# Optimization experiments

Measured on AMD Instinct MI355X. Metric: run time of the kernel, lower is better.

## Reference

```python
import jax, jax.numpy as jnp
import numpy as np

D = 256; H = 4; HD = 64; NL = 12; MAXP = 16; DIM = 8; PDIM = 4; B = 128
EPS = 1e-5
SCALE = float(np.sqrt(HD))


def _ln(x, g, b):
    m = jnp.mean(x, -1, keepdims=True)
    v = jnp.mean((x - m) ** 2, -1, keepdims=True)
    return (x - m) * jax.lax.rsqrt(v + EPS) * g + b


def _mha(xq, xkv, Wqkv, bqkv, Wo, bo, causal):
    # Wqkv is the packed PyTorch in_proj_weight [3D, D]
    Bq, S, _ = xq.shape
    K = xkv.shape[1]
    q = (xq @ Wqkv[:D].T + bqkv[:D]).reshape(Bq, S, H, HD).transpose(0, 2, 1, 3)
    k = (xkv @ Wqkv[D:2 * D].T + bqkv[D:2 * D]).reshape(Bq, K, H, HD).transpose(0, 2, 1, 3)
    v = (xkv @ Wqkv[2 * D:].T + bqkv[2 * D:]).reshape(Bq, K, H, HD).transpose(0, 2, 1, 3)
    s = jnp.einsum('bhqd,bhkd->bhqk', q, k) / SCALE
    if causal:
        s = jnp.where(jnp.tril(jnp.ones((S, K), bool)), s, -jnp.inf)
    a = jax.nn.softmax(s, -1)
    o = jnp.einsum('bhqk,bhkd->bhqd', a, v).transpose(0, 2, 1, 3).reshape(Bq, S, D)
    return o @ Wo.T + bo


def _decode(tgt, mem, p):
    # post-LN TransformerDecoder (norm_first=False), dropout in eval mode
    x = tgt
    for l in range(NL):
        x = _ln(x + _mha(x, x, p['sa_Wqkv'][l], p['sa_bqkv'][l], p['sa_Wo'][l], p['sa_bo'][l], True), p['ln1_g'][l], p['ln1_b'][l])
        x = _ln(x + _mha(x, mem, p['ca_Wqkv'][l], p['ca_bqkv'][l], p['ca_Wo'][l], p['ca_bo'][l], False), p['ln2_g'][l], p['ln2_b'][l])
        h = jax.nn.relu(x @ p['lin1_W'][l].T + p['lin1_b'][l])
        x = _ln(x + h @ p['lin2_W'][l].T + p['lin2_b'][l], p['ln3_g'][l], p['ln3_b'][l])
    return x


def _forward(U_real, U_imag, tok_W, tok_b, pos_emb, sa_Wqkv, sa_bqkv, sa_Wo, sa_bo, ca_Wqkv, ca_bqkv, ca_Wo, ca_bo, lin1_W, lin1_b, lin2_W, lin2_b, ln1_g, ln1_b, ln2_g, ln2_b, ln3_g, ln3_b, out_W, out_b, param_low, param_high):
    p = dict(sa_Wqkv=sa_Wqkv, sa_bqkv=sa_bqkv, sa_Wo=sa_Wo, sa_bo=sa_bo,
             ca_Wqkv=ca_Wqkv, ca_bqkv=ca_bqkv, ca_Wo=ca_Wo, ca_bo=ca_bo,
             lin1_W=lin1_W, lin1_b=lin1_b, lin2_W=lin2_W, lin2_b=lin2_b,
             ln1_g=ln1_g, ln1_b=ln1_b, ln2_g=ln2_g, ln2_b=ln2_b, ln3_g=ln3_g, ln3_b=ln3_b)
    Bq = U_real.shape[0]
    vec = jnp.concatenate([U_real.reshape(Bq, -1), U_imag.reshape(Bq, -1)], -1)  # [B, 2*dim^2]
    src = vec @ tok_W.T + tok_b  # [B, D]
    mem = src[:, None, :]  # [B, 1, D] cross-attn memory
    seq = [src]
    for i in range(MAXP):
        tgt = jnp.stack(seq, 1) + pos_emb[:i + 1][None]  # [B, i+1, D]
        x = _decode(tgt, mem, p)
        seq.append(x[:, -1])
    logits = jnp.stack(seq[1:], 1)  # [B, MAXP, D]
    pn = jax.nn.sigmoid(logits @ out_W.T + out_b)  # [B, MAXP, PDIM]
    return param_low + (param_high - param_low) * pn


def setup_inputs() -> dict:
    key = jax.random.key(0)
    ks = jax.random.split(key, 16)
    def w(k, shape, s=0.02):
        return jax.random.normal(k, shape, dtype=jnp.float32) * s
    return {
        'U_real': jax.random.normal(ks[0], (B, DIM, DIM), dtype=jnp.float32),
        'U_imag': jax.random.normal(ks[1], (B, DIM, DIM), dtype=jnp.float32),
        'tok_W': w(ks[2], (D, 2 * DIM * DIM)), 'tok_b': jnp.zeros((D,), jnp.float32),
        'pos_emb': w(ks[3], (MAXP + 1, D)),
        'sa_Wqkv': w(ks[4], (NL, 3 * D, D)), 'sa_bqkv': jnp.zeros((NL, 3 * D), jnp.float32),
        'sa_Wo': w(ks[5], (NL, D, D)), 'sa_bo': jnp.zeros((NL, D), jnp.float32),
        'ca_Wqkv': w(ks[6], (NL, 3 * D, D)), 'ca_bqkv': jnp.zeros((NL, 3 * D), jnp.float32),
        'ca_Wo': w(ks[7], (NL, D, D)), 'ca_bo': jnp.zeros((NL, D), jnp.float32),
        'lin1_W': w(ks[8], (NL, 4 * D, D)), 'lin1_b': jnp.zeros((NL, 4 * D), jnp.float32),
        'lin2_W': w(ks[9], (NL, D, 4 * D)), 'lin2_b': jnp.zeros((NL, D), jnp.float32),
        'ln1_g': jnp.ones((NL, D), jnp.float32), 'ln1_b': jnp.zeros((NL, D), jnp.float32),
        'ln2_g': jnp.ones((NL, D), jnp.float32), 'ln2_b': jnp.zeros((NL, D), jnp.float32),
        'ln3_g': jnp.ones((NL, D), jnp.float32), 'ln3_b': jnp.zeros((NL, D), jnp.float32),
        'out_W': w(ks[10], (PDIM, D)), 'out_b': jnp.zeros((PDIM,), jnp.float32),
        'param_low': jnp.array([-1.0, 0.0, 0.0, 0.0], jnp.float32),
        'param_high': jnp.array([1.0, 1.0, 6.2832, 1.0], jnp.float32),
    }


def reference(U_real, U_imag, tok_W, tok_b, pos_emb, sa_Wqkv, sa_bqkv, sa_Wo, sa_bo, ca_Wqkv, ca_bqkv, ca_Wo, ca_bo, lin1_W, lin1_b, lin2_W, lin2_b, ln1_g, ln1_b, ln2_g, ln2_b, ln3_g, ln3_b, out_W, out_b, param_low, param_high):
    return _forward(U_real, U_imag, tok_W, tok_b, pos_emb, sa_Wqkv, sa_bqkv, sa_Wo, sa_bo, ca_Wqkv, ca_bqkv, ca_Wo, ca_bo, lin1_W, lin1_b, lin2_W, lin2_b, ln1_g, ln1_b, ln2_g, ln2_b, ln3_g, ln3_b, out_W, out_b, param_low, param_high)
```

## Files before the change

### kernel.cpp

```cpp
#include <hip/hip_runtime.h>
#include <hip/hip_bf16.h>


typedef __attribute__((ext_vector_type(8))) short short8;
typedef __attribute__((ext_vector_type(4))) float f32x4;

#define EPS_ 1e-5f

__device__ __forceinline__ unsigned short f2b(float x){
  union { float f; unsigned u; } c; c.f = x;
  unsigned r = (c.u + 0x7fffu + ((c.u >> 16) & 1u)) >> 16;
  return (unsigned short)r;
}
__device__ __forceinline__ float b2f(unsigned short u){
  union { unsigned u; float f; } c; c.u = ((unsigned)u) << 16;
  return c.f;
}
__device__ __forceinline__ unsigned long long pack4b(const f32x4 a){
  return (unsigned long long)f2b(a[0]) |
         ((unsigned long long)f2b(a[1]) << 16) |
         ((unsigned long long)f2b(a[2]) << 32) |
         ((unsigned long long)f2b(a[3]) << 48);
}
__device__ __forceinline__ unsigned long long pack2f(float a, float b){
  union { float f; unsigned u; } x, y; x.f = a; y.f = b;
  return (unsigned long long)x.u | ((unsigned long long)y.u << 32);
}
__device__ __forceinline__ float lo_f(unsigned long long v){
  union { unsigned u; float f; } c; c.u = (unsigned)v; return c.f;
}
__device__ __forceinline__ float hi_f(unsigned long long v){
  union { unsigned u; float f; } c; c.u = (unsigned)(v >> 32); return c.f;
}

#define AL(p)    __hip_atomic_load((p),  __ATOMIC_RELAXED, __HIP_MEMORY_SCOPE_AGENT)
#define AS(p,v)  __hip_atomic_store((p), (v), __ATOMIC_RELAXED, __HIP_MEMORY_SCOPE_AGENT)

#define OFF_WQKV 0ull
#define OFF_WO   4718592ull
#define OFF_L1   6291456ull
#define OFF_L2   12582912ull
#define OFF_SRC  18874368ull
#define OFF_CC   19005440ull
#define OFF_KV   19791872ull
#define OFF_XH   44957696ull
#define OFF_ZA   45219840ull
#define OFF_ZB   45613056ull
#define OFF_FLG  46006272ull

__global__ void k_conv(const float* __restrict__ wqkv, const float* __restrict__ wo,
                       const float* __restrict__ l1, const float* __restrict__ l2,
                       unsigned short* __restrict__ dst){
  const long long n0 = 12LL*768*256;
  const long long n1 = n0 + 12LL*256*256;
  const long long n2 = n1 + 12LL*1024*256;
  const long long n3 = n2 + 12LL*256*1024;
  for (long long idx = (long long)blockIdx.x*256 + threadIdx.x; idx < n3;
       idx += (long long)gridDim.x*256){
    float v;
    if (idx < n0) v = wqkv[idx];
    else if (idx < n1) v = wo[idx - n0];
    else if (idx < n2) v = l1[idx - n1];
    else v = l2[idx - n2];
    dst[idx] = f2b(v);
  }
}

__global__ void k_src(const float* __restrict__ U_real, const float* __restrict__ U_imag,
                      const float* __restrict__ tok_W, const float* __restrict__ tok_b,
                      const float* __restrict__ pos,
                      float* __restrict__ src, float* __restrict__ xh0){
  int b = blockIdx.x, n = threadIdx.x;
  const float* w = tok_W + n*128;
  const float* ur = U_real + b*64;
  const float* ui = U_imag + b*64;
  float acc = tok_b[n];
  #pragma unroll 8
  for (int k = 0; k < 64; ++k) acc += w[k]*ur[k];
  #pragma unroll 8
  for (int k = 0; k < 64; ++k) acc += w[64+k]*ui[k];
  src[b*256+n] = acc;
  xh0[b*256+n] = acc + pos[n];
}

__global__ void k_cc(const float* __restrict__ caW, const float* __restrict__ cab,
                     const float* __restrict__ caWo, const float* __restrict__ cabo,
                     const float* __restrict__ src, unsigned short* __restrict__ cc){
  int l = blockIdx.x >> 7, b = blockIdx.x & 127, t = threadIdx.x;
  __shared__ float v[256];
  const float* s = src + b*256;
  {
    const float* w = caW + ((long long)l*768 + 512 + t)*256;
    float a = cab[l*768 + 512 + t];
    #pragma unroll 8
    for (int k = 0; k < 256; ++k) a += w[k]*s[k];
    v[t] = a;
  }
  __syncthreads();
  {
    const float* w = caWo + ((long long)l*256 + t)*256;
    float a = cabo[l*256 + t];
    #pragma unroll 8
    for (int k = 0; k < 256; ++k) a += w[k]*v[k];
    cc[((long long)l*128 + b)*256 + t] = f2b(a);
  }
}

#define PUBW(FARR) do{                                                       \
  __syncthreads();                                                           \
  if (tid == 0) AS(FARR + l*4 + h, seq);                                     \
  if (tid < 3){                                                              \
    int ho = tid + (tid >= h ? 1 : 0);                                       \
    const int* fp = FARR + l*4 + ho;                                         \
    while (AL(fp) < seq) __builtin_amdgcn_s_sleep(2);                        \
  }                                                                          \
  __syncthreads();                                                           \
}while(0)

__global__ __launch_bounds__(512, 1) void k_main(
  const unsigned short* __restrict__ wqkv,
  const unsigned short* __restrict__ wo,
  const unsigned short* __restrict__ wl1,
  const unsigned short* __restrict__ wl2,
  const float* __restrict__ bqkv, const float* __restrict__ bo_,
  const float* __restrict__ bl1,  const float* __restrict__ bl2,
  const float* __restrict__ g1, const float* __restrict__ be1,
  const float* __restrict__ g2, const float* __restrict__ be2,
  const float* __restrict__ g3, const float* __restrict__ be3,
  const unsigned short* __restrict__ cc,
  const float* __restrict__ pos,
  const float* __restrict__ outW,
  const float* __restrict__ outb,
  const float* __restrict__ plow, const float* __restrict__ phigh,
  unsigned short* __restrict__ kvc,
  unsigned long long* __restrict__ xh,
  unsigned long long* __restrict__ zA,
  unsigned long long* __restrict__ zB,
  int* __restrict__ flags,
  float* __restrict__ out)
{
  __shared__ float xf[16][260];
  __shared__ float zf[16][260];
  __shared__ float yf[16][260];
  __shared__ unsigned short xb[16][264];
  __shared__ unsigned short hs[16][264];
  __shared__ unsigned short qs[16][72];
  __shared__ unsigned short os[16][72];

  const int tid  = threadIdx.x;
  const int w    = tid >> 6, lane = tid & 63;
  const int l    = blockIdx.x >> 2;
  const int h    = blockIdx.x & 3;
  const int mrow = lane & 15, kgrp = lane >> 4;

  int* fin = flags;
  int* fA  = flags + 384;
  int* fB  = flags + 432;

  for (int t = 0; t < 16; ++t){
    for (int g = 0; g < 8; ++g){
      const int seq = t*8 + g + 1;

      {
        int need = (l == 0) ? t : (t+1);
        if (need > 0 && tid < 4){
          const int* fp = fin + (l*4 + tid)*8 + g;
          while (AL(fp) < need) __builtin_amdgcn_s_sleep(2);
        }
        __syncthreads();
        int row = tid >> 5, c8 = (tid & 31)*8;
        const unsigned long long* xp =
            xh + (((size_t)(l & 1)*8 + g)*16 + row)*128 + (c8 >> 1);
        #pragma unroll
        for (int j = 0; j < 4; ++j){
          unsigned long long v = AL(xp + j);
          float f0 = lo_f(v), f1 = hi_f(v);
          xf[row][c8+2*j]   = f0;  xf[row][c8+2*j+1] = f1;
          xb[row][c8+2*j]   = f2b(f0);
          xb[row][c8+2*j+1] = f2b(f1);
        }
      }
      __syncthreads();

      {
        short8 a[8];
        #pragma unroll
        for (int kc = 0; kc < 8; ++kc)
          a[kc] = *(const short8*)&xb[mrow][kc*32 + kgrp*8];
        const unsigned short* wl = wqkv + (size_t)l*196608;
        for (int t2 = w; t2 < 12; t2 += 8){
          int p = t2 >> 2, q4 = t2 & 3;
          int n_l = q4*16 + mrow;
          const unsigned short* wp = wl + (size_t)(p*256 + h*64 + n_l)*256 + kgrp*8;
          f32x4 acc = {0,0,0,0};
          #pragma unroll
          for (int kc = 0; kc < 8; ++kc){
            short8 b0 = *(const short8*)(wp + kc*32);
            acc = __builtin_amdgcn_mfma_f32_16x16x32_bf16(a[kc], b0, acc, 0,0,0);
          }
          float bias = bqkv[l*768 + p*256 + h*64 + n_l];
          #pragma unroll
          for (int r = 0; r < 4; ++r){
            int br = kgrp*4 + r;
            float v = acc[r] + bias;
            if (p == 0){
              qs[br][n_l] = f2b(v);
            } else {
              size_t kb = (((((size_t)l*4 + h)*8 + g)*16 + br)*16 + t)*128
                          + (p == 2 ? 64 : 0) + n_l;
              kvc[kb] = f2b(v);
            }
          }
        }
      }
      __syncthreads();

      {
        int row = w*2 + (lane >> 5);
        int lid = lane & 31;
        float q0 = b2f(qs[row][lid*2]), q1 = b2f(qs[row][lid*2+1]);
        const unsigned short* base =
            kvc + (((((size_t)l*4 + h)*8 + g)*16 + row)*16)*128 + lid*2;
        float sv[16];
        #pragma unroll
        for (int j = 0; j < 16; ++j){
          if (j <= t){
            const unsigned short* kp = base + j*128;
            float p = q0*b2f(kp[0]) + q1*b2f(kp[1]);
            p += __shfl_xor(p, 1);
            p += __shfl_xor(p, 2);
            p += __shfl_xor(p, 4);
            p += __shfl_xor(p, 8);
            p += __shfl_xor(p, 16);
            sv[j] = p * 0.125f;
          } else sv[j] = -1e30f;
        }
        float mx = sv[0];
        #pragma unroll
        for (int j = 1; j < 16; ++j) mx = fmaxf(mx, sv[j]);
        float den = 0.f, e[16];
        #pragma unroll
        for (int j = 0; j < 16; ++j){ e[j] = __expf(sv[j]-mx); den += e[j]; }
        float rd = 1.f/den;
        float o0 = 0.f, o1 = 0.f;
        #pragma unroll
        for (int j = 0; j < 16; ++j){
          if (j <= t){
            const unsigned short* vp = base + j*128 + 64;
            o0 += e[j]*b2f(vp[0]);
            o1 += e[j]*b2f(vp[1]);
          }
        }
        os[row][lid*2]   = f2b(o0*rd);
        os[row][lid*2+1] = f2b(o1*rd);
      }
      __syncthreads();

      {
        short8 a2[2];
        #pragma unroll
        for (int kc = 0; kc < 2; ++kc)
          a2[kc] = *(const short8*)&os[mrow][kc*32 + kgrp*8];
        #pragma unroll
        for (int u2 = 0; u2 < 2; ++u2){
          int n_g = (w*2+u2)*16 + mrow;
          const unsigned short* wp = wo + (size_t)l*65536 + (size_t)n_g*256 + h*64 + kgrp*8;
          f32x4 acc = {0,0,0,0};
          #pragma unroll
          for (int kc = 0; kc < 2; ++kc){
            short8 b0 = *(const short8*)(wp + kc*32);
            acc = __builtin_amdgcn_mfma_f32_16x16x32_bf16(a2[kc], b0, acc, 0,0,0);
          }
          AS(zA + ((size_t)(l*4 + h)*256 + n_g)*4 + kgrp, pack4b(acc));
        }
      }
      PUBW(fA);

      {
        int col = tid & 255, rq2 = tid >> 8;
        float a8[8] = {0,0,0,0,0,0,0,0};
        #pragma unroll
        for (int s4 = 0; s4 < 4; ++s4){
          const unsigned long long* bp = zA + ((size_t)(l*4 + s4)*256 + col)*4 + rq2*2;
          #pragma unroll
          for (int q = 0; q < 2; ++q){
            unsigned long long v = AL(bp + q);
            a8[q*4+0] += b2f((unsigned short)v);
            a8[q*4+1] += b2f((unsigned short)(v >> 16));
            a8[q*4+2] += b2f((unsigned short)(v >> 32));
            a8[q*4+3] += b2f((unsigned short)(v >> 48));
          }
        }
        float bias = bo_[l*256 + col];
        #pragma unroll
        for (int r = 0; r < 8; ++r){
          int row = rq2*8 + r;
          zf[row][col] = a8[r] + bias + xf[row][col];
        }
      }
      __syncthreads();

      {
        int row = tid >> 5, c8 = (tid & 31)*8;
        float tt[8];
        #pragma unroll
        for (int k = 0; k < 8; ++k) tt[k] = zf[row][c8+k];
        float sm = 0, sq = 0;
        #pragma unroll
        for (int k = 0; k < 8; ++k){ sm += tt[k]; sq += tt[k]*tt[k]; }
        sm += __shfl_xor(sm,1);  sq += __shfl_xor(sq,1);
        sm += __shfl_xor(sm,2);  sq += __shfl_xor(sq,2);
        sm += __shfl_xor(sm,4);  sq += __shfl_xor(sq,4);
        sm += __shfl_xor(sm,8);  sq += __shfl_xor(sq,8);
        sm += __shfl_xor(sm,16); sq += __shfl_xor(sq,16);
        float mean = sm*(1.f/256), var = sq*(1.f/256) - mean*mean;
        float rs = rsqrtf(var + EPS_);
        const float* g1p = g1 + l*256 + c8;
        const float* b1p = be1 + l*256 + c8;
        const unsigned short* ccp = cc + ((size_t)l*128 + g*16 + row)*256 + c8;
        #pragma unroll
        for (int k = 0; k < 8; ++k)
          tt[k] = (tt[k]-mean)*rs*g1p[k] + b1p[k] + b2f(ccp[k]);
        sm = 0; sq = 0;
        #pragma unroll
        for (int k = 0; k < 8; ++k){ sm += tt[k]; sq += tt[k]*tt[k]; }
        sm += __shfl_xor(sm,1);  sq += __shfl_xor(sq,1);
        sm += __shfl_xor(sm,2);  sq += __shfl_xor(sq,2);
        sm += __shfl_xor(sm,4);  sq += __shfl_xor(sq,4);
        sm += __shfl_xor(sm,8);  sq += __shfl_xor(sq,8);
        sm += __shfl_xor(sm,16); sq += __shfl_xor(sq,16);
        mean = sm*(1.f/256); var = sq*(1.f/256) - mean*mean;
        rs = rsqrtf(var + EPS_);
        const float* g2p = g2 + l*256 + c8;
        const float* b2p = be2 + l*256 + c8;
        #pragma unroll
        for (int k = 0; k < 8; ++k){
          float y = (tt[k]-mean)*rs*g2p[k] + b2p[k];
          yf[row][c8+k] = y;
          xb[row][c8+k] = f2b(y);
        }
      }
      __syncthreads();

      {
        short8 a[8];
        #pragma unroll
        for (int kc = 0; kc < 8; ++kc)
          a[kc] = *(const short8*)&xb[mrow][kc*32 + kgrp*8];
        const unsigned short* wl = wl1 + (size_t)l*262144;
        #pragma unroll
        for (int u2 = 0; u2 < 2; ++u2){
          int n_sl = (w*2+u2)*16 + mrow;
          const unsigned short* wp = wl + (size_t)(h*256 + n_sl)*256 + kgrp*8;
          f32x4 acc = {0,0,0,0};
          #pragma unroll
          for (int kc = 0; kc < 8; ++kc){
            short8 b0 = *(const short8*)(wp + kc*32);
            acc = __builtin_amdgcn_mfma_f32_16x16x32_bf16(a[kc], b0, acc, 0,0,0);
          }
          float bias = bl1[l*1024 + h*256 + n_sl];
          #pragma unroll
          for (int r = 0; r < 4; ++r){
            float hv = acc[r] + bias;
            hs[kgrp*4 + r][n_sl] = f2b(hv > 0.f ? hv : 0.f);
          }
        }
      }
      __syncthreads();

      {
        short8 ah[8];
        #pragma unroll
        for (int kc = 0; kc < 8; ++kc)
          ah[kc] = *(const short8*)&hs[mrow][kc*32 + kgrp*8];
        #pragma unroll
        for (int u2 = 0; u2 < 2; ++u2){
          int n_g = (w*2+u2)*16 + mrow;
          const unsigned short* wp = wl2 + (size_t)l*262144 + (size_t)n_g*1024 + h*256 + kgrp*8;
          f32x4 acc = {0,0,0,0};
          #pragma unroll
          for (int kc = 0; kc < 8; ++kc){
            short8 b0 = *(const short8*)(wp + kc*32);
            acc = __builtin_amdgcn_mfma_f32_16x16x32_bf16(ah[kc], b0, acc, 0,0,0);
          }
          AS(zB + ((size_t)(l*4 + h)*256 + n_g)*4 + kgrp, pack4b(acc));
        }
      }
      PUBW(fB);

      {
        int col = tid & 255, rq2 = tid >> 8;
        float a8[8] = {0,0,0,0,0,0,0,0};
        #pragma unroll
        for (int s4 = 0; s4 < 4; ++s4){
          const unsigned long long* bp = zB + ((size_t)(l*4 + s4)*256 + col)*4 + rq2*2;
          #pragma unroll
          for (int q = 0; q < 2; ++q){
            unsigned long long v = AL(bp + q);
            a8[q*4+0] += b2f((unsigned short)v);
            a8[q*4+1] += b2f((unsigned short)(v >> 16));
            a8[q*4+2] += b2f((unsigned short)(v >> 32));
            a8[q*4+3] += b2f((unsigned short)(v >> 48));
          }
        }
        float bias = bl2[l*256 + col];
        #pragma unroll
        for (int r = 0; r < 8; ++r){
          int row = rq2*8 + r;
          zf[row][col] = a8[r] + bias + yf[row][col];
        }
      }
      __syncthreads();

      {
        int row = tid >> 5, c8 = (tid & 31)*8;
        float tt[8];
        #pragma unroll
        for (int k = 0; k < 8; ++k) tt[k] = zf[row][c8+k];
        float sm = 0, sq = 0;
        #pragma unroll
        for (int k = 0; k < 8; ++k){ sm += tt[k]; sq += tt[k]*tt[k]; }
        sm += __shfl_xor(sm,1);  sq += __shfl_xor(sq,1);
        sm += __shfl_xor(sm,2);  sq += __shfl_xor(sq,2);
        sm += __shfl_xor(sm,4);  sq += __shfl_xor(sq,4);
        sm += __shfl_xor(sm,8);  sq += __shfl_xor(sq,8);
        sm += __shfl_xor(sm,16); sq += __shfl_xor(sq,16);
        float mean = sm*(1.f/256), var = sq*(1.f/256) - mean*mean;
        float rs = rsqrtf(var + EPS_);
        const float* g3p = g3 + l*256 + c8;
        const float* b3p = be3 + l*256 + c8;
        float xn[8];
        #pragma unroll
        for (int k = 0; k < 8; ++k)
          xn[k] = (tt[k]-mean)*rs*g3p[k] + b3p[k];
        if (l == 11){
          if (h == 0){
            float pr[4];
            #pragma unroll
            for (int p = 0; p < 4; ++p){
              float a = 0.f;
              #pragma unroll
              for (int k = 0; k < 8; ++k) a += xn[k]*outW[p*256 + c8 + k];
              a += __shfl_xor(a,1); a += __shfl_xor(a,2);
              a += __shfl_xor(a,4); a += __shfl_xor(a,8);
              a += __shfl_xor(a,16);
              pr[p] = a;
            }
            if ((tid & 31) == 0){
              int gr = g*16 + row;
              #pragma unroll
              for (int p = 0; p < 4; ++p){
                float v2 = pr[p] + outb[p];
                float sg = 1.f/(1.f + __expf(-v2));
                out[((size_t)gr*16 + t)*4 + p] = plow[p] + (phigh[p]-plow[p])*sg;
              }
            }
          }
          if (t < 15){
            const float* pp = pos + (t+1)*256 + c8;
            #pragma unroll
            for (int k = 0; k < 8; ++k) xn[k] += pp[k];
          }
        }
        bool last = (l == 11) && (t == 15);
        if (!last && ((c8 >> 6) == h)){
          unsigned long long* xp =
              xh + (((size_t)((l+1) & 1)*8 + g)*16 + row)*128 + (c8 >> 1);
          #pragma unroll
          for (int j = 0; j < 4; ++j)
            AS(xp + j, pack2f(xn[2*j], xn[2*j+1]));
        }
      }
      __syncthreads();
      if (!((l == 11) && (t == 15)) && tid == 0)
        AS(fin + ((((l+1) % 12)*4) + h)*8 + g, t+1);
    }
  }
}

extern "C" void kernel_launch(void* const* d_in, const int* in_sizes, int n_in,
                              void* d_out, int out_size, void* d_ws, size_t ws_size,
                              hipStream_t stream) {
  const float* U_real = (const float*)d_in[0];
  const float* U_imag = (const float*)d_in[1];
  const float* tok_W  = (const float*)d_in[2];
  const float* tok_b  = (const float*)d_in[3];
  const float* pos    = (const float*)d_in[4];
  const float* saW    = (const float*)d_in[5];
  const float* sab    = (const float*)d_in[6];
  const float* saWo   = (const float*)d_in[7];
  const float* sabo   = (const float*)d_in[8];
  const float* caW    = (const float*)d_in[9];
  const float* cab    = (const float*)d_in[10];
  const float* caWo   = (const float*)d_in[11];
  const float* cabo   = (const float*)d_in[12];
  const float* l1W    = (const float*)d_in[13];
  const float* l1b    = (const float*)d_in[14];
  const float* l2W    = (const float*)d_in[15];
  const float* l2b    = (const float*)d_in[16];
  const float* g1     = (const float*)d_in[17];
  const float* be1    = (const float*)d_in[18];
  const float* g2     = (const float*)d_in[19];
  const float* be2    = (const float*)d_in[20];
  const float* g3     = (const float*)d_in[21];
  const float* be3    = (const float*)d_in[22];
  const float* outW   = (const float*)d_in[23];
  const float* outb   = (const float*)d_in[24];
  const float* plow   = (const float*)d_in[25];
  const float* phigh  = (const float*)d_in[26];

  char* ws = (char*)d_ws;
  unsigned short* wb        = (unsigned short*)(ws + OFF_WQKV);
  float* srcb               = (float*)(ws + OFF_SRC);
  unsigned short* ccb       = (unsigned short*)(ws + OFF_CC);
  unsigned short* kvc       = (unsigned short*)(ws + OFF_KV);
  unsigned long long* xhb   = (unsigned long long*)(ws + OFF_XH);
  unsigned long long* zAb   = (unsigned long long*)(ws + OFF_ZA);
  unsigned long long* zBb   = (unsigned long long*)(ws + OFF_ZB);
  int* flags                = (int*)(ws + OFF_FLG);

  (void)hipMemsetAsync(ws + OFF_FLG, 0, 4096, stream);
  k_conv<<<dim3(4608), dim3(256), 0, stream>>>(saW, saWo, l1W, l2W, wb);
  k_src<<<dim3(128), dim3(256), 0, stream>>>(U_real, U_imag, tok_W, tok_b, pos,
                                             srcb, (float*)xhb);
  k_cc<<<dim3(1536), dim3(256), 0, stream>>>(caW, cab, caWo, cabo, srcb, ccb);
  k_main<<<dim3(48), dim3(512), 0, stream>>>(
      wb,
      (unsigned short*)(ws + OFF_WO),
      (unsigned short*)(ws + OFF_L1),
      (unsigned short*)(ws + OFF_L2),
      sab, sabo, l1b, l2b,
      g1, be1, g2, be2, g3, be3,
      ccb, pos, outW, outb, plow, phigh,
      kvc, xhb, zAb, zBb, flags, (float*)d_out);
}
```

Baseline: 4.761 ms.

## Preload per-block weight fragments into registers and shorten spin-wait sleeps

Each block now loads its Wo, lin1 and lin2 weight fragments and the lin1 bias into registers once, before the token loop. The 128 iterations then reuse them instead of re-reading from global memory/cache each time. The spin-wait sleep is shortened, and the flag publish for the next layer is moved ahead of the output-head writes, so downstream blocks are released sooner. The register cost rises sharply (about 36 short8 values per thread), which risks spills under the 512-thread launch bound.

```diff
diff --git a/kernel.cpp b/kernel.cpp
--- a/kernel.cpp
+++ b/kernel.cpp
@@ -112,7 +112,7 @@
   if (tid < 3){                                                              \
     int ho = tid + (tid >= h ? 1 : 0);                                       \
     const int* fp = FARR + l*4 + ho;                                         \
-    while (AL(fp) < seq) __builtin_amdgcn_s_sleep(2);                        \
+    while (AL(fp) < seq) __builtin_amdgcn_s_sleep(1);                        \
   }                                                                          \
   __syncthreads();                                                           \
 }while(0)
@@ -157,6 +157,25 @@
   int* fA  = flags + 384;
   int* fB  = flags + 432;
 
+  short8 wWo[2][2], wL1[2][8], wL2[2][8];
+  float bL1r[2];
+  {
+    #pragma unroll
+    for (int u = 0; u < 2; ++u){
+      int n_g = (w*2+u)*16 + mrow;
+      const unsigned short* p1 = wo + (size_t)l*65536 + (size_t)n_g*256 + h*64 + kgrp*8;
+      #pragma unroll
+      for (int kc = 0; kc < 2; ++kc) wWo[u][kc] = *(const short8*)(p1 + kc*32);
+      const unsigned short* p2 = wl1 + (size_t)l*262144 + (size_t)(h*256 + n_g)*256 + kgrp*8;
+      #pragma unroll
+      for (int kc = 0; kc < 8; ++kc) wL1[u][kc] = *(const short8*)(p2 + kc*32);
+      bL1r[u] = bl1[l*1024 + h*256 + n_g];
+      const unsigned short* p3 = wl2 + (size_t)l*262144 + (size_t)n_g*1024 + h*256 + kgrp*8;
+      #pragma unroll
+      for (int kc = 0; kc < 8; ++kc) wL2[u][kc] = *(const short8*)(p3 + kc*32);
+    }
+  }
+
   for (int t = 0; t < 16; ++t){
     for (int g = 0; g < 8; ++g){
       const int seq = t*8 + g + 1;
@@ -165,7 +184,7 @@
         int need = (l == 0) ? t : (t+1);
         if (need > 0 && tid < 4){
           const int* fp = fin + (l*4 + tid)*8 + g;
-          while (AL(fp) < need) __builtin_amdgcn_s_sleep(2);
+          while (AL(fp) < need) __builtin_amdgcn_s_sleep(1);
         }
         __syncthreads();
         int row = tid >> 5, c8 = (tid & 31)*8;
@@ -264,13 +283,10 @@
         #pragma unroll
         for (int u2 = 0; u2 < 2; ++u2){
           int n_g = (w*2+u2)*16 + mrow;
-          const unsigned short* wp = wo + (size_t)l*65536 + (size_t)n_g*256 + h*64 + kgrp*8;
           f32x4 acc = {0,0,0,0};
           #pragma unroll
-          for (int kc = 0; kc < 2; ++kc){
-            short8 b0 = *(const short8*)(wp + kc*32);
-            acc = __builtin_amdgcn_mfma_f32_16x16x32_bf16(a2[kc], b0, acc, 0,0,0);
-          }
+          for (int kc = 0; kc < 2; ++kc)
+            acc = __builtin_amdgcn_mfma_f32_16x16x32_bf16(a2[kc], wWo[u2][kc], acc, 0,0,0);
           AS(zA + ((size_t)(l*4 + h)*256 + n_g)*4 + kgrp, pack4b(acc));
         }
       }
@@ -347,18 +363,14 @@
         #pragma unroll
         for (int kc = 0; kc < 8; ++kc)
           a[kc] = *(const short8*)&xb[mrow][kc*32 + kgrp*8];
-        const unsigned short* wl = wl1 + (size_t)l*262144;
         #pragma unroll
         for (int u2 = 0; u2 < 2; ++u2){
           int n_sl = (w*2+u2)*16 + mrow;
-          const unsigned short* wp = wl + (size_t)(h*256 + n_sl)*256 + kgrp*8;
           f32x4 acc = {0,0,0,0};
           #pragma unroll
-          for (int kc = 0; kc < 8; ++kc){
-            short8 b0 = *(const short8*)(wp + kc*32);
-            acc = __builtin_amdgcn_mfma_f32_16x16x32_bf16(a[kc], b0, acc, 0,0,0);
-          }
-          float bias = bl1[l*1024 + h*256 + n_sl];
+          for (int kc = 0; kc < 8; ++kc)
+            acc = __builtin_amdgcn_mfma_f32_16x16x32_bf16(a[kc], wL1[u2][kc], acc, 0,0,0);
+          float bias = bL1r[u2];
           #pragma unroll
           for (int r = 0; r < 4; ++r){
             float hv = acc[r] + bias;
@@ -376,13 +388,10 @@
         #pragma unroll
         for (int u2 = 0; u2 < 2; ++u2){
           int n_g = (w*2+u2)*16 + mrow;
-          const unsigned short* wp = wl2 + (size_t)l*262144 + (size_t)n_g*1024 + h*256 + kgrp*8;
           f32x4 acc = {0,0,0,0};
           #pragma unroll
-          for (int kc = 0; kc < 8; ++kc){
-            short8 b0 = *(const short8*)(wp + kc*32);
-            acc = __builtin_amdgcn_mfma_f32_16x16x32_bf16(ah[kc], b0, acc, 0,0,0);
-          }
+          for (int kc = 0; kc < 8; ++kc)
+            acc = __builtin_amdgcn_mfma_f32_16x16x32_bf16(ah[kc], wL2[u2][kc], acc, 0,0,0);
           AS(zB + ((size_t)(l*4 + h)*256 + n_g)*4 + kgrp, pack4b(acc));
         }
       }
@@ -433,36 +442,27 @@
         #pragma unroll
         for (int k = 0; k < 8; ++k)
           xn[k] = (tt[k]-mean)*rs*g3p[k] + b3p[k];
-        if (l == 11){
-          if (h == 0){
-            float pr[4];
+
+        float pr[4] = {0,0,0,0};
+        const bool doHead = (l == 11) && (h == 0);
+        if (doHead){
+          #pragma unroll
+          for (int p = 0; p < 4; ++p){
+            float a = 0.f;
             #pragma unroll
-            for (int p = 0; p < 4; ++p){
-              float a = 0.f;
-              #pragma unroll
-              for (int k = 0; k < 8; ++k) a += xn[k]*outW[p*256 + c8 + k];
-              a += __shfl_xor(a,1); a += __shfl_xor(a,2);
-              a += __shfl_xor(a,4); a += __shfl_xor(a,8);
-              a += __shfl_xor(a,16);
-              pr[p] = a;
-            }
-            if ((tid & 31) == 0){
-              int gr = g*16 + row;
-              #pragma unroll
-              for (int p = 0; p < 4; ++p){
-                float v2 = pr[p] + outb[p];
-                float sg = 1.f/(1.f + __expf(-v2));
-                out[((size_t)gr*16 + t)*4 + p] = plow[p] + (phigh[p]-plow[p])*sg;
-              }
-            }
-          }
-          if (t < 15){
-            const float* pp = pos + (t+1)*256 + c8;
-            #pragma unroll
-            for (int k = 0; k < 8; ++k) xn[k] += pp[k];
-          }
-        }
-        bool last = (l == 11) && (t == 15);
+            for (int k = 0; k < 8; ++k) a += xn[k]*outW[p*256 + c8 + k];
+            a += __shfl_xor(a,1); a += __shfl_xor(a,2);
+            a += __shfl_xor(a,4); a += __shfl_xor(a,8);
+            a += __shfl_xor(a,16);
+            pr[p] = a;
+          }
+        }
+        if (l == 11 && t < 15){
+          const float* pp = pos + (t+1)*256 + c8;
+          #pragma unroll
+          for (int k = 0; k < 8; ++k) xn[k] += pp[k];
+        }
+        const bool last = (l == 11) && (t == 15);
         if (!last && ((c8 >> 6) == h)){
           unsigned long long* xp =
               xh + (((size_t)((l+1) & 1)*8 + g)*16 + row)*128 + (c8 >> 1);
@@ -470,10 +470,19 @@
           for (int j = 0; j < 4; ++j)
             AS(xp + j, pack2f(xn[2*j], xn[2*j+1]));
         }
-      }
-      __syncthreads();
-      if (!((l == 11) && (t == 15)) && tid == 0)
-        AS(fin + ((((l+1) % 12)*4) + h)*8 + g, t+1);
+        __syncthreads();
+        if (!last && tid == 0)
+          AS(fin + ((((l+1) % 12)*4) + h)*8 + g, t+1);
+        if (doHead && ((tid & 31) == 0)){
+          int gr = g*16 + row;
+          #pragma unroll
+          for (int p = 0; p < 4; ++p){
+            float v2 = pr[p] + outb[p];
+            float sg = 1.f/(1.f + __expf(-v2));
+            out[((size_t)gr*16 + t)*4 + p] = plow[p] + (phigh[p]-plow[p])*sg;
+          }
+        }
+      }
     }
   }
 }
```

Result: no change. 4.780 ms (+0.4%).

## Run one 1024-thread block per layer instead of four head-split blocks

Applied to the files above, without the earlier changes.

The persistent pipelined decoder kernel moves from 48 blocks (layer × head, 512 threads) to 12 blocks (one per layer, 1024 threads), each computing all heads and the full Wo/FFN matmuls locally. This drops the cross-block partial-sum exchange through global memory (zA/zB buffers) and the PUBW spin barriers between the four head blocks of a layer. The cost is that each layer now runs on one CU, so per-token matmul work is no longer spread over four CUs and far fewer CUs are busy. The attention, LayerNorm and KV-cache indexing are re-tiled for the 16-wave layout.

```diff
diff --git a/kernel.cpp b/kernel.cpp
--- a/kernel.cpp
+++ b/kernel.cpp
@@ -15,12 +15,6 @@
 __device__ __forceinline__ float b2f(unsigned short u){
   union { unsigned u; float f; } c; c.u = ((unsigned)u) << 16;
   return c.f;
-}
-__device__ __forceinline__ unsigned long long pack4b(const f32x4 a){
-  return (unsigned long long)f2b(a[0]) |
-         ((unsigned long long)f2b(a[1]) << 16) |
-         ((unsigned long long)f2b(a[2]) << 32) |
-         ((unsigned long long)f2b(a[3]) << 48);
 }
 __device__ __forceinline__ unsigned long long pack2f(float a, float b){
   union { float f; unsigned u; } x, y; x.f = a; y.f = b;
@@ -44,8 +38,6 @@
 #define OFF_CC   19005440ull
 #define OFF_KV   19791872ull
 #define OFF_XH   44957696ull
-#define OFF_ZA   45219840ull
-#define OFF_ZB   45613056ull
 #define OFF_FLG  46006272ull
 
 __global__ void k_conv(const float* __restrict__ wqkv, const float* __restrict__ wo,
@@ -106,18 +98,7 @@
   }
 }
 
-#define PUBW(FARR) do{                                                       \
-  __syncthreads();                                                           \
-  if (tid == 0) AS(FARR + l*4 + h, seq);                                     \
-  if (tid < 3){                                                              \
-    int ho = tid + (tid >= h ? 1 : 0);                                       \
-    const int* fp = FARR + l*4 + ho;                                         \
-    while (AL(fp) < seq) __builtin_amdgcn_s_sleep(2);                        \
-  }                                                                          \
-  __syncthreads();                                                           \
-}while(0)
-
-__global__ __launch_bounds__(512, 1) void k_main(
+__global__ __launch_bounds__(1024, 1) void k_main(
   const unsigned short* __restrict__ wqkv,
   const unsigned short* __restrict__ wo,
   const unsigned short* __restrict__ wl1,
@@ -134,8 +115,6 @@
   const float* __restrict__ plow, const float* __restrict__ phigh,
   unsigned short* __restrict__ kvc,
   unsigned long long* __restrict__ xh,
-  unsigned long long* __restrict__ zA,
-  unsigned long long* __restrict__ zB,
   int* __restrict__ flags,
   float* __restrict__ out)
 {
@@ -143,42 +122,43 @@
   __shared__ float zf[16][260];
   __shared__ float yf[16][260];
   __shared__ unsigned short xb[16][264];
-  __shared__ unsigned short hs[16][264];
-  __shared__ unsigned short qs[16][72];
-  __shared__ unsigned short os[16][72];
+  __shared__ unsigned short qs[16][264];
+  __shared__ unsigned short os[16][264];
+  __shared__ unsigned short hs[16][1032];
 
   const int tid  = threadIdx.x;
   const int w    = tid >> 6, lane = tid & 63;
-  const int l    = blockIdx.x >> 2;
-  const int h    = blockIdx.x & 3;
+  const int l    = blockIdx.x;
   const int mrow = lane & 15, kgrp = lane >> 4;
-
   int* fin = flags;
-  int* fA  = flags + 384;
-  int* fB  = flags + 432;
+
+  const unsigned short* wqkv_l = wqkv + (size_t)l*196608;
+  const unsigned short* wo_l   = wo   + (size_t)l*65536;
+  const unsigned short* wl1_l  = wl1  + (size_t)l*262144;
+  const unsigned short* wl2_l  = wl2  + (size_t)l*262144;
+  unsigned short* kvc_l        = kvc  + (size_t)l*1048576;
+  const int prev = (l == 0) ? 11 : (l-1);
 
   for (int t = 0; t < 16; ++t){
     for (int g = 0; g < 8; ++g){
-      const int seq = t*8 + g + 1;
-
       {
         int need = (l == 0) ? t : (t+1);
-        if (need > 0 && tid < 4){
-          const int* fp = fin + (l*4 + tid)*8 + g;
-          while (AL(fp) < need) __builtin_amdgcn_s_sleep(2);
+        if (need > 0 && tid == 0){
+          const int* fp = fin + prev*8 + g;
+          while (AL(fp) < need) __builtin_amdgcn_s_sleep(1);
         }
         __syncthreads();
-        int row = tid >> 5, c8 = (tid & 31)*8;
+        int row = w;
         const unsigned long long* xp =
-            xh + (((size_t)(l & 1)*8 + g)*16 + row)*128 + (c8 >> 1);
-        #pragma unroll
-        for (int j = 0; j < 4; ++j){
-          unsigned long long v = AL(xp + j);
-          float f0 = lo_f(v), f1 = hi_f(v);
-          xf[row][c8+2*j]   = f0;  xf[row][c8+2*j+1] = f1;
-          xb[row][c8+2*j]   = f2b(f0);
-          xb[row][c8+2*j+1] = f2b(f1);
-        }
+            xh + ((size_t)(l & 1)*8 + g)*2048 + (size_t)row*128 + lane*2;
+        unsigned long long v0 = AL(xp);
+        unsigned long long v1 = AL(xp + 1);
+        int c4 = lane*4;
+        float f0 = lo_f(v0), f1 = hi_f(v0), f2 = lo_f(v1), f3 = hi_f(v1);
+        xf[row][c4]   = f0; xf[row][c4+1] = f1;
+        xf[row][c4+2] = f2; xf[row][c4+3] = f3;
+        xb[row][c4]   = f2b(f0); xb[row][c4+1] = f2b(f1);
+        xb[row][c4+2] = f2b(f2); xb[row][c4+3] = f2b(f3);
       }
       __syncthreads();
 
@@ -187,28 +167,27 @@
         #pragma unroll
         for (int kc = 0; kc < 8; ++kc)
           a[kc] = *(const short8*)&xb[mrow][kc*32 + kgrp*8];
-        const unsigned short* wl = wqkv + (size_t)l*196608;
-        for (int t2 = w; t2 < 12; t2 += 8){
-          int p = t2 >> 2, q4 = t2 & 3;
-          int n_l = q4*16 + mrow;
-          const unsigned short* wp = wl + (size_t)(p*256 + h*64 + n_l)*256 + kgrp*8;
+        #pragma unroll
+        for (int p = 0; p < 3; ++p){
+          int n_g = w*16 + mrow;
+          const unsigned short* wp = wqkv_l + (size_t)(p*256 + n_g)*256 + kgrp*8;
           f32x4 acc = {0,0,0,0};
           #pragma unroll
           for (int kc = 0; kc < 8; ++kc){
             short8 b0 = *(const short8*)(wp + kc*32);
             acc = __builtin_amdgcn_mfma_f32_16x16x32_bf16(a[kc], b0, acc, 0,0,0);
           }
-          float bias = bqkv[l*768 + p*256 + h*64 + n_l];
+          float bias = bqkv[l*768 + p*256 + n_g];
+          int head = n_g >> 6, d = n_g & 63;
           #pragma unroll
           for (int r = 0; r < 4; ++r){
             int br = kgrp*4 + r;
             float v = acc[r] + bias;
             if (p == 0){
-              qs[br][n_l] = f2b(v);
+              qs[br][n_g] = f2b(v);
             } else {
-              size_t kb = (((((size_t)l*4 + h)*8 + g)*16 + br)*16 + t)*128
-                          + (p == 2 ? 64 : 0) + n_l;
-              kvc[kb] = f2b(v);
+              kvc_l[(((size_t)(g*16+br)*4 + head)*16 + t)*128
+                    + (p == 2 ? 64 : 0) + d] = f2b(v);
             }
           }
         }
@@ -216,22 +195,26 @@
       __syncthreads();
 
       {
-        int row = w*2 + (lane >> 5);
-        int lid = lane & 31;
-        float q0 = b2f(qs[row][lid*2]), q1 = b2f(qs[row][lid*2+1]);
+        int task = tid >> 4;
+        int row = task & 15, head = task >> 4;
+        int lid = tid & 15;
+        float q4[4];
+        #pragma unroll
+        for (int u = 0; u < 4; ++u) q4[u] = b2f(qs[row][head*64 + lid*4 + u]);
         const unsigned short* base =
-            kvc + (((((size_t)l*4 + h)*8 + g)*16 + row)*16)*128 + lid*2;
+            kvc_l + (((size_t)(g*16+row)*4 + head)*16)*128 + lid*4;
         float sv[16];
         #pragma unroll
         for (int j = 0; j < 16; ++j){
           if (j <= t){
             const unsigned short* kp = base + j*128;
-            float p = q0*b2f(kp[0]) + q1*b2f(kp[1]);
+            float p = 0.f;
+            #pragma unroll
+            for (int u = 0; u < 4; ++u) p += q4[u]*b2f(kp[u]);
             p += __shfl_xor(p, 1);
             p += __shfl_xor(p, 2);
             p += __shfl_xor(p, 4);
             p += __shfl_xor(p, 8);
-            p += __shfl_xor(p, 16);
             sv[j] = p * 0.125f;
           } else sv[j] = -1e30f;
         }
@@ -242,102 +225,84 @@
         #pragma unroll
         for (int j = 0; j < 16; ++j){ e[j] = __expf(sv[j]-mx); den += e[j]; }
         float rd = 1.f/den;
-        float o0 = 0.f, o1 = 0.f;
+        float o4[4] = {0,0,0,0};
         #pragma unroll
         for (int j = 0; j < 16; ++j){
           if (j <= t){
             const unsigned short* vp = base + j*128 + 64;
-            o0 += e[j]*b2f(vp[0]);
-            o1 += e[j]*b2f(vp[1]);
-          }
-        }
-        os[row][lid*2]   = f2b(o0*rd);
-        os[row][lid*2+1] = f2b(o1*rd);
-      }
-      __syncthreads();
-
-      {
-        short8 a2[2];
-        #pragma unroll
-        for (int kc = 0; kc < 2; ++kc)
-          a2[kc] = *(const short8*)&os[mrow][kc*32 + kgrp*8];
-        #pragma unroll
-        for (int u2 = 0; u2 < 2; ++u2){
-          int n_g = (w*2+u2)*16 + mrow;
-          const unsigned short* wp = wo + (size_t)l*65536 + (size_t)n_g*256 + h*64 + kgrp*8;
-          f32x4 acc = {0,0,0,0};
-          #pragma unroll
-          for (int kc = 0; kc < 2; ++kc){
-            short8 b0 = *(const short8*)(wp + kc*32);
-            acc = __builtin_amdgcn_mfma_f32_16x16x32_bf16(a2[kc], b0, acc, 0,0,0);
-          }
-          AS(zA + ((size_t)(l*4 + h)*256 + n_g)*4 + kgrp, pack4b(acc));
-        }
-      }
-      PUBW(fA);
-
-      {
-        int col = tid & 255, rq2 = tid >> 8;
-        float a8[8] = {0,0,0,0,0,0,0,0};
-        #pragma unroll
-        for (int s4 = 0; s4 < 4; ++s4){
-          const unsigned long long* bp = zA + ((size_t)(l*4 + s4)*256 + col)*4 + rq2*2;
-          #pragma unroll
-          for (int q = 0; q < 2; ++q){
-            unsigned long long v = AL(bp + q);
-            a8[q*4+0] += b2f((unsigned short)v);
-            a8[q*4+1] += b2f((unsigned short)(v >> 16));
-            a8[q*4+2] += b2f((unsigned short)(v >> 32));
-            a8[q*4+3] += b2f((unsigned short)(v >> 48));
-          }
-        }
-        float bias = bo_[l*256 + col];
-        #pragma unroll
-        for (int r = 0; r < 8; ++r){
-          int row = rq2*8 + r;
-          zf[row][col] = a8[r] + bias + xf[row][col];
-        }
-      }
-      __syncthreads();
-
-      {
-        int row = tid >> 5, c8 = (tid & 31)*8;
-        float tt[8];
-        #pragma unroll
-        for (int k = 0; k < 8; ++k) tt[k] = zf[row][c8+k];
+            float ej = e[j];
+            #pragma unroll
+            for (int u = 0; u < 4; ++u) o4[u] += ej*b2f(vp[u]);
+          }
+        }
+        #pragma unroll
+        for (int u = 0; u < 4; ++u)
+          os[row][head*64 + lid*4 + u] = f2b(o4[u]*rd);
+      }
+      __syncthreads();
+
+      {
+        short8 a[8];
+        #pragma unroll
+        for (int kc = 0; kc < 8; ++kc)
+          a[kc] = *(const short8*)&os[mrow][kc*32 + kgrp*8];
+        int n_g = w*16 + mrow;
+        const unsigned short* wp = wo_l + (size_t)n_g*256 + kgrp*8;
+        f32x4 acc = {0,0,0,0};
+        #pragma unroll
+        for (int kc = 0; kc < 8; ++kc){
+          short8 b0 = *(const short8*)(wp + kc*32);
+          acc = __builtin_amdgcn_mfma_f32_16x16x32_bf16(a[kc], b0, acc, 0,0,0);
+        }
+        float bias = bo_[l*256 + n_g];
+        #pragma unroll
+        for (int r = 0; r < 4; ++r){
+          int br = kgrp*4 + r;
+          zf[br][n_g] = acc[r] + bias + xf[br][n_g];
+        }
+      }
+      __syncthreads();
+
+      {
+        int row = w, c4 = lane*4;
+        float tt[4];
+        #pragma unroll
+        for (int k = 0; k < 4; ++k) tt[k] = zf[row][c4+k];
         float sm = 0, sq = 0;
         #pragma unroll
-        for (int k = 0; k < 8; ++k){ sm += tt[k]; sq += tt[k]*tt[k]; }
+        for (int k = 0; k < 4; ++k){ sm += tt[k]; sq += tt[k]*tt[k]; }
         sm += __shfl_xor(sm,1);  sq += __shfl_xor(sq,1);
         sm += __shfl_xor(sm,2);  sq += __shfl_xor(sq,2);
         sm += __shfl_xor(sm,4);  sq += __shfl_xor(sq,4);
         sm += __shfl_xor(sm,8);  sq += __shfl_xor(sq,8);
         sm += __shfl_xor(sm,16); sq += __shfl_xor(sq,16);
+        sm += __shfl_xor(sm,32); sq += __shfl_xor(sq,32);
         float mean = sm*(1.f/256), var = sq*(1.f/256) - mean*mean;
         float rs = rsqrtf(var + EPS_);
-        const float* g1p = g1 + l*256 + c8;
-        const float* b1p = be1 + l*256 + c8;
-        const unsigned short* ccp = cc + ((size_t)l*128 + g*16 + row)*256 + c8;
-        #pragma unroll
-        for (int k = 0; k < 8; ++k)
+        const float* g1p = g1 + l*256 + c4;
+        const float* b1p = be1 + l*256 + c4;
+        const unsigned short* ccp = cc + ((size_t)l*128 + g*16 + row)*256 + c4;
+        #pragma unroll
+        for (int k = 0; k < 4; ++k)
           tt[k] = (tt[k]-mean)*rs*g1p[k] + b1p[k] + b2f(ccp[k]);
         sm = 0; sq = 0;
         #pragma unroll
-        for (int k = 0; k < 8; ++k){ sm += tt[k]; sq += tt[k]*tt[k]; }
+        for (int k = 0; k < 4; ++k){ sm += tt[k]; sq += tt[k]*tt[k]; }
         sm += __shfl_xor(sm,1);  sq += __shfl_xor(sq,1);
         sm += __shfl_xor(sm,2);  sq += __shfl_xor(sq,2);
         sm += __shfl_xor(sm,4);  sq += __shfl_xor(sq,4);
         sm += __shfl_xor(sm,8);  sq += __shfl_xor(sq,8);
         sm += __shfl_xor(sm,16); sq += __shfl_xor(sq,16);
+        sm += __shfl_xor(sm,32); sq += __shfl_xor(sq,32);
         mean = sm*(1.f/256); var = sq*(1.f/256) - mean*mean;
         rs = rsqrtf(var + EPS_);
-        const float* g2p = g2 + l*256 + c8;
-        const float* b2p = be2 + l*256 + c8;
-        #pragma unroll
-        for (int k = 0; k < 8; ++k){
+        const float* g2p = g2 + l*256 + c4;
+        const float* b2p = be2 + l*256 + c4;
+        #pragma unroll
+        for (int k = 0; k < 4; ++k){
           float y = (tt[k]-mean)*rs*g2p[k] + b2p[k];
-          yf[row][c8+k] = y;
-          xb[row][c8+k] = f2b(y);
+          yf[row][c4+k] = y;
+          xb[row][c4+k] = f2b(y);
         }
       }
       __syncthreads();
@@ -347,133 +312,107 @@
         #pragma unroll
         for (int kc = 0; kc < 8; ++kc)
           a[kc] = *(const short8*)&xb[mrow][kc*32 + kgrp*8];
-        const unsigned short* wl = wl1 + (size_t)l*262144;
-        #pragma unroll
-        for (int u2 = 0; u2 < 2; ++u2){
-          int n_sl = (w*2+u2)*16 + mrow;
-          const unsigned short* wp = wl + (size_t)(h*256 + n_sl)*256 + kgrp*8;
+        #pragma unroll
+        for (int u = 0; u < 4; ++u){
+          int n_g = (w + 16*u)*16 + mrow;
+          const unsigned short* wp = wl1_l + (size_t)n_g*256 + kgrp*8;
           f32x4 acc = {0,0,0,0};
           #pragma unroll
           for (int kc = 0; kc < 8; ++kc){
             short8 b0 = *(const short8*)(wp + kc*32);
             acc = __builtin_amdgcn_mfma_f32_16x16x32_bf16(a[kc], b0, acc, 0,0,0);
           }
-          float bias = bl1[l*1024 + h*256 + n_sl];
+          float bias = bl1[l*1024 + n_g];
           #pragma unroll
           for (int r = 0; r < 4; ++r){
             float hv = acc[r] + bias;
-            hs[kgrp*4 + r][n_sl] = f2b(hv > 0.f ? hv : 0.f);
-          }
-        }
-      }
-      __syncthreads();
-
-      {
-        short8 ah[8];
-        #pragma unroll
-        for (int kc = 0; kc < 8; ++kc)
-          ah[kc] = *(const short8*)&hs[mrow][kc*32 + kgrp*8];
-        #pragma unroll
-        for (int u2 = 0; u2 < 2; ++u2){
-          int n_g = (w*2+u2)*16 + mrow;
-          const unsigned short* wp = wl2 + (size_t)l*262144 + (size_t)n_g*1024 + h*256 + kgrp*8;
-          f32x4 acc = {0,0,0,0};
-          #pragma unroll
-          for (int kc = 0; kc < 8; ++kc){
-            short8 b0 = *(const short8*)(wp + kc*32);
-            acc = __builtin_amdgcn_mfma_f32_16x16x32_bf16(ah[kc], b0, acc, 0,0,0);
-          }
-          AS(zB + ((size_t)(l*4 + h)*256 + n_g)*4 + kgrp, pack4b(acc));
-        }
-      }
-      PUBW(fB);
-
-      {
-        int col = tid & 255, rq2 = tid >> 8;
-        float a8[8] = {0,0,0,0,0,0,0,0};
-        #pragma unroll
-        for (int s4 = 0; s4 < 4; ++s4){
-          const unsigned long long* bp = zB + ((size_t)(l*4 + s4)*256 + col)*4 + rq2*2;
-          #pragma unroll
-          for (int q = 0; q < 2; ++q){
-            unsigned long long v = AL(bp + q);
-            a8[q*4+0] += b2f((unsigned short)v);
-            a8[q*4+1] += b2f((unsigned short)(v >> 16));
-            a8[q*4+2] += b2f((unsigned short)(v >> 32));
-            a8[q*4+3] += b2f((unsigned short)(v >> 48));
-          }
-        }
-        float bias = bl2[l*256 + col];
-        #pragma unroll
-        for (int r = 0; r < 8; ++r){
-          int row = rq2*8 + r;
-          zf[row][col] = a8[r] + bias + yf[row][col];
-        }
-      }
-      __syncthreads();
-
-      {
-        int row = tid >> 5, c8 = (tid & 31)*8;
-        float tt[8];
-        #pragma unroll
-        for (int k = 0; k < 8; ++k) tt[k] = zf[row][c8+k];
+            hs[kgrp*4 + r][n_g] = f2b(hv > 0.f ? hv : 0.f);
+          }
+        }
+      }
+      __syncthreads();
+
+      {
+        int n_g = w*16 + mrow;
+        const unsigned short* wp = wl2_l + (size_t)n_g*1024 + kgrp*8;
+        f32x4 acc = {0,0,0,0};
+        #pragma unroll
+        for (int kc = 0; kc < 32; ++kc){
+          short8 a = *(const short8*)&hs[mrow][kc*32 + kgrp*8];
+          short8 b0 = *(const short8*)(wp + kc*32);
+          acc = __builtin_amdgcn_mfma_f32_16x16x32_bf16(a, b0, acc, 0,0,0);
+        }
+        float bias = bl2[l*256 + n_g];
+        #pragma unroll
+        for (int r = 0; r < 4; ++r){
+          int br = kgrp*4 + r;
+          zf[br][n_g] = acc[r] + bias + yf[br][n_g];
+        }
+      }
+      __syncthreads();
+
+      {
+        int row = w, c4 = lane*4;
+        float tt[4];
+        #pragma unroll
+        for (int k = 0; k < 4; ++k) tt[k] = zf[row][c4+k];
         float sm = 0, sq = 0;
         #pragma unroll
-        for (int k = 0; k < 8; ++k){ sm += tt[k]; sq += tt[k]*tt[k]; }
+        for (int k = 0; k < 4; ++k){ sm += tt[k]; sq += tt[k]*tt[k]; }
         sm += __shfl_xor(sm,1);  sq += __shfl_xor(sq,1);
         sm += __shfl_xor(sm,2);  sq += __shfl_xor(sq,2);
         sm += __shfl_xor(sm,4);  sq += __shfl_xor(sq,4);
         sm += __shfl_xor(sm,8);  sq += __shfl_xor(sq,8);
         sm += __shfl_xor(sm,16); sq += __shfl_xor(sq,16);
+        sm += __shfl_xor(sm,32); sq += __shfl_xor(sq,32);
         float mean = sm*(1.f/256), var = sq*(1.f/256) - mean*mean;
         float rs = rsqrtf(var + EPS_);
-        const float* g3p = g3 + l*256 + c8;
-        const float* b3p = be3 + l*256 + c8;
-        float xn[8];
-        #pragma unroll
-        for (int k = 0; k < 8; ++k)
+        const float* g3p = g3 + l*256 + c4;
+        const float* b3p = be3 + l*256 + c4;
+        float xn[4];
+        #pragma unroll
+        for (int k = 0; k < 4; ++k)
           xn[k] = (tt[k]-mean)*rs*g3p[k] + b3p[k];
-        if (l == 11){
-          if (h == 0){
-            float pr[4];
+
+        float pr[4] = {0,0,0,0};
+        const bool doHead = (l == 11);
+        if (doHead){
+          #pragma unroll
+          for (int p = 0; p < 4; ++p){
+            float a = 0.f;
             #pragma unroll
-            for (int p = 0; p < 4; ++p){
-              float a = 0.f;
-              #pragma unroll
-              for (int k = 0; k < 8; ++k) a += xn[k]*outW[p*256 + c8 + k];
-              a += __shfl_xor(a,1); a += __shfl_xor(a,2);
-              a += __shfl_xor(a,4); a += __shfl_xor(a,8);
-              a += __shfl_xor(a,16);
-              pr[p] = a;
-            }
-            if ((tid & 31) == 0){
-              int gr = g*16 + row;
-              #pragma unroll
-              for (int p = 0; p < 4; ++p){
-                float v2 = pr[p] + outb[p];
-                float sg = 1.f/(1.f + __expf(-v2));
-                out[((size_t)gr*16 + t)*4 + p] = plow[p] + (phigh[p]-plow[p])*sg;
-              }
-            }
+            for (int k = 0; k < 4; ++k) a += xn[k]*outW[p*256 + c4 + k];
+            a += __shfl_xor(a,1); a += __shfl_xor(a,2);
+            a += __shfl_xor(a,4); a += __shfl_xor(a,8);
+            a += __shfl_xor(a,16); a += __shfl_xor(a,32);
+            pr[p] = a;
           }
           if (t < 15){
-            const float* pp = pos + (t+1)*256 + c8;
+            const float* pp = pos + (t+1)*256 + c4;
             #pragma unroll
-            for (int k = 0; k < 8; ++k) xn[k] += pp[k];
-          }
-        }
-        bool last = (l == 11) && (t == 15);
-        if (!last && ((c8 >> 6) == h)){
+            for (int k = 0; k < 4; ++k) xn[k] += pp[k];
+          }
+        }
+        const bool last = (l == 11) && (t == 15);
+        if (!last){
           unsigned long long* xp =
-              xh + (((size_t)((l+1) & 1)*8 + g)*16 + row)*128 + (c8 >> 1);
-          #pragma unroll
-          for (int j = 0; j < 4; ++j)
-            AS(xp + j, pack2f(xn[2*j], xn[2*j+1]));
-        }
-      }
-      __syncthreads();
-      if (!((l == 11) && (t == 15)) && tid == 0)
-        AS(fin + ((((l+1) % 12)*4) + h)*8 + g, t+1);
+              xh + ((size_t)((l+1) & 1)*8 + g)*2048 + (size_t)row*128 + lane*2;
+          AS(xp,     pack2f(xn[0], xn[1]));
+          AS(xp + 1, pack2f(xn[2], xn[3]));
+        }
+        __syncthreads();
+        if (!last && tid == 0)
+          AS(fin + l*8 + g, t+1);
+        if (doHead && lane == 0){
+          int gr = g*16 + row;
+          #pragma unroll
+          for (int p = 0; p < 4; ++p){
+            float v2 = pr[p] + outb[p];
+            float sg = 1.f/(1.f + __expf(-v2));
+            out[((size_t)gr*16 + t)*4 + p] = plow[p] + (phigh[p]-plow[p])*sg;
+          }
+        }
+      }
     }
   }
 }
@@ -515,16 +454,14 @@
   unsigned short* ccb       = (unsigned short*)(ws + OFF_CC);
   unsigned short* kvc       = (unsigned short*)(ws + OFF_KV);
   unsigned long long* xhb   = (unsigned long long*)(ws + OFF_XH);
-  unsigned long long* zAb   = (unsigned long long*)(ws + OFF_ZA);
-  unsigned long long* zBb   = (unsigned long long*)(ws + OFF_ZB);
   int* flags                = (int*)(ws + OFF_FLG);
 
-  (void)hipMemsetAsync(ws + OFF_FLG, 0, 4096, stream);
+  (void)hipMemsetAsync(ws + OFF_FLG, 0, 512, stream);
   k_conv<<<dim3(4608), dim3(256), 0, stream>>>(saW, saWo, l1W, l2W, wb);
   k_src<<<dim3(128), dim3(256), 0, stream>>>(U_real, U_imag, tok_W, tok_b, pos,
                                              srcb, (float*)xhb);
   k_cc<<<dim3(1536), dim3(256), 0, stream>>>(caW, cab, caWo, cabo, srcb, ccb);
-  k_main<<<dim3(48), dim3(512), 0, stream>>>(
+  k_main<<<dim3(12), dim3(1024), 0, stream>>>(
       wb,
       (unsigned short*)(ws + OFF_WO),
       (unsigned short*)(ws + OFF_L1),
@@ -532,5 +469,5 @@
       sab, sabo, l1b, l2b,
       g1, be1, g2, be2, g3, be3,
       ccb, pos, outW, outb, plow, phigh,
-      kvc, xhb, zAb, zBb, flags, (float*)d_out);
-}
+      kvc, xhb, flags, (float*)d_out);
+}
```

Measured after the change: 10.39 ms. 2.18x slower.
